# Optimization experiments

Hardware: AMD Instinct MI355X
Metric: run time of the kernel (lower is better)

## Reference

```python
import math
import jax, jax.numpy as jnp
import numpy as np

N = 256                      # 'n' from __init__
LMAX = 15
NSH = (LMAX + 1) ** 2        # number of SH coefficients = 256
A = 2 * N                    # alpha grid size
B = N - 4                    # beta grid size (linspace(0,pi,n)[2:-2])
K = 1024                     # fixed max number of peaks per projection (jit-compatible capacity)
THR = 2.0 * math.pi / N      # dedup distance threshold


def _rot_zyz(a, b, c):
    def rz(t):
        return np.array([[math.cos(t), -math.sin(t), 0.0],
                         [math.sin(t),  math.cos(t), 0.0],
                         [0.0, 0.0, 1.0]])
    def ry(t):
        return np.array([[math.cos(t), 0.0, math.sin(t)],
                         [0.0, 1.0, 0.0],
                         [-math.sin(t), 0.0, math.cos(t)]])
    return rz(a) @ ry(b) @ rz(c)


def _grid_xyz(R):
    a = np.linspace(0.0, 2.0 * math.pi, A)
    b = np.linspace(0.0, math.pi, N)[2:-2]
    AA, BB = np.meshgrid(a, b, indexing='ij')       # [A, B]
    xyz = np.stack([np.sin(BB) * np.cos(AA),
                    np.sin(BB) * np.sin(AA),
                    np.cos(BB)], axis=-1)            # [A, B, 3]
    return (xyz @ R.T).astype(np.float32)


def setup_inputs() -> dict:
    key = jax.random.key(0)
    k1, k2, k3 = jax.random.split(key, 3)
    signal = jax.random.normal(k1, (NSH,), dtype=jnp.float32)
    # Precomputed SH projection buffers (fixed tensors in the torch module);
    # random stand-ins preserve the exact compute pattern of the einsum.
    sh1 = jax.random.normal(k2, (NSH, A, B), dtype=jnp.float32) * 0.1
    sh2 = jax.random.normal(k3, (NSH, A, B), dtype=jnp.float32) * 0.1
    xyz1 = jnp.asarray(_grid_xyz(_rot_zyz(math.pi / 2, math.pi / 2, math.pi / 2)))
    xyz2 = jnp.asarray(_grid_xyz(np.eye(3)))
    return {"signal": signal, "sh1": sh1, "sh2": sh2, "xyz1": xyz1, "xyz2": xyz2}


def _detect_peaks(signal, sh, xyz):
    # f[a,b] = sum_i signal[i] * sh[i,a,b]   (memory-bound GEMV over the grid)
    f = jnp.einsum('i,iab->ab', signal, sh)                       # [A, B]
    # strict local maxima along beta (rows) and alpha (columns); interior only
    row = jnp.pad((f[:, 1:-1] > f[:, :-2]) & (f[:, 1:-1] > f[:, 2:]),
                  ((0, 0), (1, 1)))
    col = jnp.pad((f[1:-1, :] > f[:-2, :]) & (f[1:-1, :] > f[2:, :]),
                  ((1, 1), (0, 0)))
    mask = (row & col).reshape(-1)                                # [A*B]
    ff = f.reshape(-1)
    score = jnp.where(mask, ff, -jnp.inf)
    _, idx = jax.lax.top_k(score, K)                              # fixed-capacity peak set
    valid = jnp.take(mask, idx)
    radius = jnp.where(valid, jnp.take(ff, idx), 0.0)             # [K]
    peaks = jnp.where(valid[:, None],
                      jnp.take(xyz.reshape(-1, 3), idx, axis=0), 0.0)  # [K, 3]
    return peaks, radius, valid


def reference(signal, sh1, sh2, xyz1, xyz2):
    p1, r1, v1 = _detect_peaks(signal, sh1, xyz1)
    p2, r2, v2 = _detect_peaks(signal, sh2, xyz2)
    # suppress peaks1 that lie within THR of any valid peak2
    d = jnp.linalg.norm(p1[:, None, :] - p2[None, :, :], axis=-1)  # [K, K]
    close = (d < THR) & v1[:, None] & v2[None, :]
    keep1 = v1 & ~jnp.any(close, axis=1)
    peaks = jnp.concatenate([jnp.where(keep1[:, None], p1, 0.0), p2], axis=0)   # [2K, 3]
    radius = jnp.concatenate([jnp.where(keep1, r1, 0.0), r2], axis=0)           # [2K]
    valid = jnp.concatenate([keep1, v2], axis=0)                                 # [2K]
    return peaks, radius, valid
```

## Files before the change

### kernel.cpp

```cpp
#include <hip/hip_runtime.h>
#include <hip/hip_bf16.h>
#include <stdint.h>

#define NSH 256
#define AG 512
#define BG 252
#define AB (AG*BG)
#define KK 1024
#define SENT 0xFFFFFFFFFFFFFFFFull

static __device__ __forceinline__ unsigned int fkey(float v){
    unsigned int u = __float_as_uint(v);
    u ^= (u >> 31) ? 0xFFFFFFFFu : 0x80000000u;
    return u;
}

__global__ __launch_bounds__(256) void k_gemv(const float* __restrict__ sig,
        const float* __restrict__ sh1, const float* __restrict__ sh2,
        float* __restrict__ f, unsigned int* __restrict__ counts){
    __shared__ float sig_s[NSH];
    int tid = threadIdx.x;
    if (blockIdx.x == 0 && blockIdx.y == 0 && tid < 2) counts[tid] = 0;
    sig_s[tid] = sig[tid];
    __syncthreads();
    int proj = blockIdx.y;
    const float* sh = proj ? sh2 : sh1;
    size_t j4 = ((size_t)blockIdx.x * 256 + tid) * 4;
    const float* p = sh + j4;
    float a0 = 0.f, a1 = 0.f, a2 = 0.f, a3 = 0.f;
    float4 buf[16];
    for (int c = 0; c < NSH; c += 16){
        #pragma unroll
        for (int u = 0; u < 16; ++u)
            buf[u] = *reinterpret_cast<const float4*>(p + (size_t)(c + u) * AB);
        __builtin_amdgcn_sched_barrier(0);
        #pragma unroll
        for (int u = 0; u < 16; ++u){
            float si = sig_s[c + u];
            a0 = fmaf(si, buf[u].x, a0);
            a1 = fmaf(si, buf[u].y, a1);
            a2 = fmaf(si, buf[u].z, a2);
            a3 = fmaf(si, buf[u].w, a3);
        }
        __builtin_amdgcn_sched_barrier(0);
    }
    float4 o; o.x = a0; o.y = a1; o.z = a2; o.w = a3;
    *reinterpret_cast<float4*>(f + (size_t)proj * AB + j4) = o;
}

__global__ __launch_bounds__(256) void k_mask(const float* __restrict__ f,
        unsigned long long* __restrict__ cand, unsigned int* __restrict__ counts){
    int proj = blockIdx.y;
    const float* fp = f + (size_t)proj * AB;
    int j = blockIdx.x * 256 + threadIdx.x;
    bool pred = false;
    unsigned long long key = 0;
    {
        int a = j / BG, b = j - a * BG;
        if (a > 0 && a < AG - 1 && b > 0 && b < BG - 1){
            float v = fp[j];
            pred = (v > fp[j-1]) && (v > fp[j+1]) && (v > fp[j-BG]) && (v > fp[j+BG]);
            if (pred)
                key = (((unsigned long long)(~fkey(v))) << 32) | (unsigned int)j;
        }
    }
    unsigned long long bal = __ballot(pred);
    if (bal){
        int lane = threadIdx.x & 63;
        int leader = __ffsll(bal) - 1;
        unsigned int base = 0;
        if (lane == leader) base = atomicAdd(&counts[proj], (unsigned int)__popcll(bal));
        base = __shfl(base, leader);
        if (pred){
            unsigned int off = (unsigned int)__popcll(bal & ((1ull << lane) - 1ull));
            cand[(size_t)proj * AB + base + off] = key;
        }
    }
}

__global__ __launch_bounds__(1024) void k_select(const unsigned long long* __restrict__ cand,
        const unsigned int* __restrict__ counts, unsigned long long* __restrict__ sel){
    int proj = blockIdx.y;
    const unsigned long long* cp = cand + (size_t)proj * AB;
    unsigned long long* sp = sel + proj * KK;
    unsigned int count = counts[proj];
    int tid = threadIdx.x;
    if (count <= KK){
        if (tid < KK) sp[tid] = SENT;
        if (tid < (int)count) sp[tid] = cp[tid];
        return;
    }
    __shared__ unsigned int hist[256];
    __shared__ unsigned int sbin, sremk;
    unsigned long long prefix = 0, pmask = 0;
    unsigned int remk = KK;
    for (int lvl = 7; lvl >= 0; --lvl){
        int shft = lvl * 8;
        if (tid < 256) hist[tid] = 0;
        __syncthreads();
        for (unsigned int i = tid; i < count; i += 1024){
            unsigned long long k = cp[i];
            if ((k & pmask) == prefix)
                atomicAdd(&hist[(unsigned int)(k >> shft) & 255u], 1u);
        }
        __syncthreads();
        if (tid < 64){
            unsigned int b0 = hist[tid*4+0], b1 = hist[tid*4+1];
            unsigned int b2 = hist[tid*4+2], b3 = hist[tid*4+3];
            unsigned int lsum = b0 + b1 + b2 + b3;
            unsigned int incl = lsum;
            #pragma unroll
            for (int off = 1; off < 64; off <<= 1){
                unsigned int v = __shfl_up(incl, off);
                if (tid >= off) incl += v;
            }
            unsigned int excl = incl - lsum;
            if (excl < remk && remk <= incl){
                unsigned int r = remk - excl;
                unsigned int c0 = b0, c01 = b0 + b1, c012 = b0 + b1 + b2;
                unsigned int bin, rr;
                if (r <= c0){ bin = tid*4+0; rr = r; }
                else if (r <= c01){ bin = tid*4+1; rr = r - c0; }
                else if (r <= c012){ bin = tid*4+2; rr = r - c01; }
                else { bin = tid*4+3; rr = r - c012; }
                sbin = bin; sremk = rr;
            }
        }
        __syncthreads();
        prefix |= ((unsigned long long)sbin) << shft;
        pmask  |= 0xFFull << shft;
        remk = sremk;
        __syncthreads();
    }
    __shared__ unsigned int pos;
    if (tid == 0) pos = 0;
    __syncthreads();
    for (unsigned int i = tid; i < count; i += 1024){
        unsigned long long k = cp[i];
        if (k <= prefix){
            unsigned int p = atomicAdd(&pos, 1u);
            sp[p] = k;
        }
    }
}

__global__ __launch_bounds__(1024) void k_sortgather(const unsigned long long* __restrict__ sel,
        const float* __restrict__ f, const float* __restrict__ xyz1,
        const float* __restrict__ xyz2, float4* __restrict__ pr,
        unsigned int* __restrict__ vb, float* __restrict__ out){
    int proj = blockIdx.y;
    int tid = threadIdx.x;
    __shared__ unsigned long long s[KK];
    s[tid] = sel[proj * KK + tid];
    __syncthreads();
    for (int k = 2; k <= KK; k <<= 1){
        for (int j = k >> 1; j > 0; j >>= 1){
            int ixj = tid ^ j;
            if (ixj > tid){
                unsigned long long a = s[tid], b = s[ixj];
                bool asc = (tid & k) == 0;
                if ((a > b) == asc){ s[tid] = b; s[ixj] = a; }
            }
            __syncthreads();
        }
    }
    unsigned long long key = s[tid];
    bool val = (key != SENT);
    unsigned int j = (unsigned int)key;
    const float* fp = f + (size_t)proj * AB;
    const float* xyz = proj ? xyz2 : xyz1;
    float4 o = make_float4(0.f, 0.f, 0.f, 0.f);
    if (val){
        o.x = xyz[(size_t)j * 3 + 0];
        o.y = xyz[(size_t)j * 3 + 1];
        o.z = xyz[(size_t)j * 3 + 2];
        o.w = fp[j];
    }
    pr[proj * KK + tid] = o;
    vb[proj * KK + tid] = val ? 1u : 0u;
    if (proj == 1){
        int row = KK + tid;
        out[row * 3 + 0] = o.x;
        out[row * 3 + 1] = o.y;
        out[row * 3 + 2] = o.z;
        out[2 * KK * 3 + row] = o.w;
        out[2 * KK * 3 + 2 * KK + row] = val ? 1.0f : 0.0f;
    }
}

__global__ __launch_bounds__(256) void k_dedup(const float4* __restrict__ pr,
        const unsigned int* __restrict__ vb, float* __restrict__ out){
    const float THRF = (float)(6.283185307179586 / 256.0);
    int tid = threadIdx.x;
    __shared__ float sx[KK], sy[KK], sz[KK];
    #pragma unroll
    for (int t = 0; t < 4; ++t){
        int idx = t * 256 + tid;
        float4 v = pr[KK + idx];
        bool v2 = vb[KK + idx] != 0;
        sx[idx] = v2 ? v.x : 1e9f;
        sy[idx] = v2 ? v.y : 1e9f;
        sz[idx] = v2 ? v.z : 1e9f;
    }
    __syncthreads();
    int k = blockIdx.x * 256 + tid;
    float4 m = pr[k];
    bool close = false;
    {
        #pragma clang fp contract(off)
        #pragma unroll 8
        for (int jj = 0; jj < KK; ++jj){
            float dx = m.x - sx[jj];
            float dy = m.y - sy[jj];
            float dz = m.z - sz[jj];
            float d2 = dx * dx + dy * dy + dz * dz;
            close = close | (sqrtf(d2) < THRF);
        }
    }
    bool keep = (vb[k] != 0) && !close;
    out[k * 3 + 0] = keep ? m.x : 0.0f;
    out[k * 3 + 1] = keep ? m.y : 0.0f;
    out[k * 3 + 2] = keep ? m.z : 0.0f;
    out[2 * KK * 3 + k] = keep ? m.w : 0.0f;
    out[2 * KK * 3 + 2 * KK + k] = keep ? 1.0f : 0.0f;
}

extern "C" void kernel_launch(void* const* d_in, const int* in_sizes, int n_in,
                              void* d_out, int out_size, void* d_ws, size_t ws_size,
                              hipStream_t stream){
    const float* sig  = (const float*)d_in[0];
    const float* sh1  = (const float*)d_in[1];
    const float* sh2  = (const float*)d_in[2];
    const float* xyz1 = (const float*)d_in[3];
    const float* xyz2 = (const float*)d_in[4];
    float* out = (float*)d_out;
    char* ws = (char*)d_ws;

    float* f                  = (float*)(ws);
    unsigned long long* cand  = (unsigned long long*)(ws + 0x100000);
    unsigned int* counts      = (unsigned int*)(ws + 0x300000);
    unsigned long long* sel   = (unsigned long long*)(ws + 0x300100);
    float4* pr                = (float4*)(ws + 0x310000);
    unsigned int* vb          = (unsigned int*)(ws + 0x320000);

    k_gemv<<<dim3(AB / 1024, 2), dim3(256), 0, stream>>>(sig, sh1, sh2, f, counts);
    k_mask<<<dim3(AB / 256, 2), dim3(256), 0, stream>>>(f, cand, counts);
    k_select<<<dim3(1, 2), dim3(1024), 0, stream>>>(cand, counts, sel);
    k_sortgather<<<dim3(1, 2), dim3(1024), 0, stream>>>(sel, f, xyz1, xyz2, pr, vb, out);
    k_dedup<<<dim3(4, 1), dim3(256), 0, stream>>>(pr, vb, out);
}
```

Before: 214.9 us.

## Stream GEMV through LDS with async global loads; fuse select and sort kernels

The GEMV now uses 128-thread blocks that keep a 16-deep ring of async global_load_lds transfers in flight, with one scalar output per thread, replacing register-buffered float4 loads. The radix select stops after four byte levels, resolves ties at the cutoff with a small insertion sort, and is fused with the bitonic sort/gather kernel, dropping one launch and the intermediate buffer. Dedup switches to 8 blocks of 128 threads. Risks include the hand-written waitcnt ordering, clamped redundant tail loads, and tie handling capped at 256 equal high-word keys.

Measured after the change: 195.6 us. -8.9%, faster.

```diff
diff --git a/kernel.cpp b/kernel.cpp
--- a/kernel.cpp
+++ b/kernel.cpp
@@ -7,7 +7,11 @@
 #define BG 252
 #define AB (AG*BG)
 #define KK 1024
+#define DEPTH 16
 #define SENT 0xFFFFFFFFFFFFFFFFull
+
+typedef float f32x4 __attribute__((ext_vector_type(4)));
+typedef __attribute__((address_space(3))) float lds_f;
 
 static __device__ __forceinline__ unsigned int fkey(float v){
     unsigned int u = __float_as_uint(v);
@@ -15,37 +19,66 @@
     return u;
 }
 
-__global__ __launch_bounds__(256) void k_gemv(const float* __restrict__ sig,
+#define GLOAD4(gp, lp) __builtin_amdgcn_global_load_lds( \
+    (__attribute__((address_space(1))) void*)(gp), \
+    (__attribute__((address_space(3))) void*)(lp), 4, 0, 0)
+
+__global__ __launch_bounds__(128) void k_gemv(const float* __restrict__ sig,
         const float* __restrict__ sh1, const float* __restrict__ sh2,
         float* __restrict__ f, unsigned int* __restrict__ counts){
     __shared__ float sig_s[NSH];
+    __shared__ float tile[DEPTH][128];
     int tid = threadIdx.x;
     if (blockIdx.x == 0 && blockIdx.y == 0 && tid < 2) counts[tid] = 0;
     sig_s[tid] = sig[tid];
+    sig_s[tid + 128] = sig[tid + 128];
     __syncthreads();
     int proj = blockIdx.y;
-    const float* sh = proj ? sh2 : sh1;
-    size_t j4 = ((size_t)blockIdx.x * 256 + tid) * 4;
-    const float* p = sh + j4;
-    float a0 = 0.f, a1 = 0.f, a2 = 0.f, a3 = 0.f;
-    float4 buf[16];
-    for (int c = 0; c < NSH; c += 16){
-        #pragma unroll
-        for (int u = 0; u < 16; ++u)
-            buf[u] = *reinterpret_cast<const float4*>(p + (size_t)(c + u) * AB);
-        __builtin_amdgcn_sched_barrier(0);
-        #pragma unroll
-        for (int u = 0; u < 16; ++u){
-            float si = sig_s[c + u];
-            a0 = fmaf(si, buf[u].x, a0);
-            a1 = fmaf(si, buf[u].y, a1);
-            a2 = fmaf(si, buf[u].z, a2);
-            a3 = fmaf(si, buf[u].w, a3);
-        }
-        __builtin_amdgcn_sched_barrier(0);
-    }
-    float4 o; o.x = a0; o.y = a1; o.z = a2; o.w = a3;
-    *reinterpret_cast<float4*>(f + (size_t)proj * AB + j4) = o;
+    const float* shp = proj ? sh2 : sh1;
+    int jbase = blockIdx.x * 128;
+    int wave = tid >> 6;
+    const float* gcol = shp + jbase + tid;
+    lds_f* wr0 = (lds_f*)&tile[0][wave * 64];
+    lds_f* rd0 = (lds_f*)&tile[0][0] + tid;
+    lds_f* sg0 = (lds_f*)&sig_s[0];
+
+    #pragma unroll
+    for (int d = 0; d < DEPTH; ++d)
+        GLOAD4(gcol + (size_t)d * AB, wr0 + d * 128);
+
+    const float* gpf  = gcol + (size_t)DEPTH * AB;
+    const float* gmax = gcol + (size_t)(NSH - 1) * AB;
+    float acc = 0.f;
+
+#define GSTEP(u, sv) do{ \
+        float v; \
+        asm volatile("s_waitcnt vmcnt(15)\n\tds_read_b32 %0, %1\n\ts_waitcnt lgkmcnt(0)" \
+            : "=v"(v) : "v"(rd0 + (u) * 128) : "memory"); \
+        acc = fmaf(sv, v, acc); \
+        const float* guse = gpf > gmax ? gmax : gpf; \
+        GLOAD4(guse, wr0 + (u) * 128); \
+        gpf += AB; \
+    }while(0)
+
+    for (int c = 0; c < 16; ++c){
+        f32x4 s0, s1, s2, s3;
+        asm volatile("ds_read_b128 %0, %4\n\t"
+                     "ds_read_b128 %1, %4 offset:16\n\t"
+                     "ds_read_b128 %2, %4 offset:32\n\t"
+                     "ds_read_b128 %3, %4 offset:48\n\t"
+                     "s_waitcnt lgkmcnt(0)"
+            : "=v"(s0), "=v"(s1), "=v"(s2), "=v"(s3)
+            : "v"(sg0 + c * 16) : "memory");
+        GSTEP(0,  s0[0]); GSTEP(1,  s0[1]); GSTEP(2,  s0[2]); GSTEP(3,  s0[3]);
+        GSTEP(4,  s1[0]); GSTEP(5,  s1[1]); GSTEP(6,  s1[2]); GSTEP(7,  s1[3]);
+        GSTEP(8,  s2[0]); GSTEP(9,  s2[1]); GSTEP(10, s2[2]); GSTEP(11, s2[3]);
+        GSTEP(12, s3[0]); GSTEP(13, s3[1]); GSTEP(14, s3[2]); GSTEP(15, s3[3]);
+    }
+#undef GSTEP
+
+    asm volatile("s_waitcnt vmcnt(0)" ::: "memory");
+    __builtin_amdgcn_sched_barrier(0);
+    f[(size_t)proj * AB + jbase + tid] = acc;
 }
 
 __global__ __launch_bounds__(256) void k_mask(const float* __restrict__ f,
@@ -78,80 +111,83 @@
     }
 }
 
-__global__ __launch_bounds__(1024) void k_select(const unsigned long long* __restrict__ cand,
-        const unsigned int* __restrict__ counts, unsigned long long* __restrict__ sel){
+__global__ __launch_bounds__(1024) void k_selsort(const unsigned long long* __restrict__ cand,
+        const unsigned int* __restrict__ counts, const float* __restrict__ f,
+        const float* __restrict__ xyz1, const float* __restrict__ xyz2,
+        float4* __restrict__ pr, unsigned int* __restrict__ vb, float* __restrict__ out){
     int proj = blockIdx.y;
     const unsigned long long* cp = cand + (size_t)proj * AB;
-    unsigned long long* sp = sel + proj * KK;
     unsigned int count = counts[proj];
     int tid = threadIdx.x;
+    __shared__ unsigned long long s[KK];
+    __shared__ unsigned int hist[256];
+    __shared__ unsigned int sbin, sremk, pos, eqn;
+    __shared__ unsigned long long eq[256];
+
     if (count <= KK){
-        if (tid < KK) sp[tid] = SENT;
-        if (tid < (int)count) sp[tid] = cp[tid];
-        return;
-    }
-    __shared__ unsigned int hist[256];
-    __shared__ unsigned int sbin, sremk;
-    unsigned long long prefix = 0, pmask = 0;
-    unsigned int remk = KK;
-    for (int lvl = 7; lvl >= 0; --lvl){
-        int shft = lvl * 8;
-        if (tid < 256) hist[tid] = 0;
+        s[tid] = (tid < (int)count) ? cp[tid] : SENT;
+    } else {
+        unsigned long long prefix = 0, pmask = 0;
+        unsigned int remk = KK;
+        for (int lvl = 7; lvl >= 4; --lvl){
+            int shft = lvl * 8;
+            if (tid < 256) hist[tid] = 0;
+            __syncthreads();
+            for (unsigned int i = tid; i < count; i += 1024){
+                unsigned long long k = cp[i];
+                if ((k & pmask) == prefix)
+                    atomicAdd(&hist[(unsigned int)(k >> shft) & 255u], 1u);
+            }
+            __syncthreads();
+            if (tid < 64){
+                unsigned int b0 = hist[tid*4+0], b1 = hist[tid*4+1];
+                unsigned int b2 = hist[tid*4+2], b3 = hist[tid*4+3];
+                unsigned int lsum = b0 + b1 + b2 + b3;
+                unsigned int incl = lsum;
+                #pragma unroll
+                for (int off = 1; off < 64; off <<= 1){
+                    unsigned int v = __shfl_up(incl, off);
+                    if (tid >= off) incl += v;
+                }
+                unsigned int excl = incl - lsum;
+                if (excl < remk && remk <= incl){
+                    unsigned int r = remk - excl;
+                    unsigned int c0 = b0, c01 = b0 + b1, c012 = b0 + b1 + b2;
+                    unsigned int bin, rr;
+                    if (r <= c0){ bin = tid*4+0; rr = r; }
+                    else if (r <= c01){ bin = tid*4+1; rr = r - c0; }
+                    else if (r <= c012){ bin = tid*4+2; rr = r - c01; }
+                    else { bin = tid*4+3; rr = r - c012; }
+                    sbin = bin; sremk = rr;
+                }
+            }
+            __syncthreads();
+            prefix |= ((unsigned long long)sbin) << shft;
+            pmask  |= 0xFFull << shft;
+            remk = sremk;
+            __syncthreads();
+        }
+        if (tid == 0){ pos = 0; eqn = 0; }
         __syncthreads();
+        unsigned int cutv = (unsigned int)(prefix >> 32);
         for (unsigned int i = tid; i < count; i += 1024){
             unsigned long long k = cp[i];
-            if ((k & pmask) == prefix)
-                atomicAdd(&hist[(unsigned int)(k >> shft) & 255u], 1u);
+            unsigned int hv = (unsigned int)(k >> 32);
+            if (hv < cutv){ s[atomicAdd(&pos, 1u)] = k; }
+            else if (hv == cutv){ unsigned e = atomicAdd(&eqn, 1u); if (e < 256) eq[e] = k; }
         }
         __syncthreads();
-        if (tid < 64){
-            unsigned int b0 = hist[tid*4+0], b1 = hist[tid*4+1];
-            unsigned int b2 = hist[tid*4+2], b3 = hist[tid*4+3];
-            unsigned int lsum = b0 + b1 + b2 + b3;
-            unsigned int incl = lsum;
-            #pragma unroll
-            for (int off = 1; off < 64; off <<= 1){
-                unsigned int v = __shfl_up(incl, off);
-                if (tid >= off) incl += v;
-            }
-            unsigned int excl = incl - lsum;
-            if (excl < remk && remk <= incl){
-                unsigned int r = remk - excl;
-                unsigned int c0 = b0, c01 = b0 + b1, c012 = b0 + b1 + b2;
-                unsigned int bin, rr;
-                if (r <= c0){ bin = tid*4+0; rr = r; }
-                else if (r <= c01){ bin = tid*4+1; rr = r - c0; }
-                else if (r <= c012){ bin = tid*4+2; rr = r - c01; }
-                else { bin = tid*4+3; rr = r - c012; }
-                sbin = bin; sremk = rr;
-            }
-        }
-        __syncthreads();
-        prefix |= ((unsigned long long)sbin) << shft;
-        pmask  |= 0xFFull << shft;
-        remk = sremk;
-        __syncthreads();
-    }
-    __shared__ unsigned int pos;
-    if (tid == 0) pos = 0;
-    __syncthreads();
-    for (unsigned int i = tid; i < count; i += 1024){
-        unsigned long long k = cp[i];
-        if (k <= prefix){
-            unsigned int p = atomicAdd(&pos, 1u);
-            sp[p] = k;
-        }
-    }
-}
-
-__global__ __launch_bounds__(1024) void k_sortgather(const unsigned long long* __restrict__ sel,
-        const float* __restrict__ f, const float* __restrict__ xyz1,
-        const float* __restrict__ xyz2, float4* __restrict__ pr,
-        unsigned int* __restrict__ vb, float* __restrict__ out){
-    int proj = blockIdx.y;
-    int tid = threadIdx.x;
-    __shared__ unsigned long long s[KK];
-    s[tid] = sel[proj * KK + tid];
+        if (tid == 0){
+            unsigned e = eqn > 256u ? 256u : eqn;
+            for (unsigned a = 1; a < e; ++a){
+                unsigned long long kx = eq[a]; int b = (int)a - 1;
+                while (b >= 0 && eq[b] > kx){ eq[b+1] = eq[b]; --b; }
+                eq[b+1] = kx;
+            }
+            unsigned take = sremk > e ? e : sremk;
+            for (unsigned r = 0; r < take; ++r) s[pos + r] = eq[r];
+        }
+    }
     __syncthreads();
     for (int k = 2; k <= KK; k <<= 1){
         for (int j = k >> 1; j > 0; j >>= 1){
@@ -188,14 +224,14 @@
     }
 }
 
-__global__ __launch_bounds__(256) void k_dedup(const float4* __restrict__ pr,
+__global__ __launch_bounds__(128) void k_dedup(const float4* __restrict__ pr,
         const unsigned int* __restrict__ vb, float* __restrict__ out){
     const float THRF = (float)(6.283185307179586 / 256.0);
     int tid = threadIdx.x;
     __shared__ float sx[KK], sy[KK], sz[KK];
     #pragma unroll
-    for (int t = 0; t < 4; ++t){
-        int idx = t * 256 + tid;
+    for (int t = 0; t < 8; ++t){
+        int idx = t * 128 + tid;
         float4 v = pr[KK + idx];
         bool v2 = vb[KK + idx] != 0;
         sx[idx] = v2 ? v.x : 1e9f;
@@ -203,7 +239,7 @@
         sz[idx] = v2 ? v.z : 1e9f;
     }
     __syncthreads();
-    int k = blockIdx.x * 256 + tid;
+    int k = blockIdx.x * 128 + tid;
     float4 m = pr[k];
     bool close = false;
     {
@@ -239,13 +275,11 @@
     float* f                  = (float*)(ws);
     unsigned long long* cand  = (unsigned long long*)(ws + 0x100000);
     unsigned int* counts      = (unsigned int*)(ws + 0x300000);
-    unsigned long long* sel   = (unsigned long long*)(ws + 0x300100);
     float4* pr                = (float4*)(ws + 0x310000);
     unsigned int* vb          = (unsigned int*)(ws + 0x320000);
 
-    k_gemv<<<dim3(AB / 1024, 2), dim3(256), 0, stream>>>(sig, sh1, sh2, f, counts);
+    k_gemv<<<dim3(AB / 128, 2), dim3(128), 0, stream>>>(sig, sh1, sh2, f, counts);
     k_mask<<<dim3(AB / 256, 2), dim3(256), 0, stream>>>(f, cand, counts);
-    k_select<<<dim3(1, 2), dim3(1024), 0, stream>>>(cand, counts, sel);
-    k_sortgather<<<dim3(1, 2), dim3(1024), 0, stream>>>(sel, f, xyz1, xyz2, pr, vb, out);
-    k_dedup<<<dim3(4, 1), dim3(256), 0, stream>>>(pr, vb, out);
-}
+    k_selsort<<<dim3(1, 2), dim3(1024), 0, stream>>>(cand, counts, f, xyz1, xyz2, pr, vb, out);
+    k_dedup<<<dim3(8, 1), dim3(128), 0, stream>>>(pr, vb, out);
+}
```
